# Performance work log

Hardware: AMD Instinct MI355X
Metric: run time of the kernel (lower is better)

The kernel has to match this reference:

```python
import jax, jax.numpy as jnp
import numpy as np

AVG_NOBJ = 49.0
NEG_SLOPE = 0.01  # torch leaky_relu default


def eops_1_to_2(x, nobj, aggregation):
    """x: [B,N,C] -> [B,C,5,N,N] equivariant basis (rank-1 -> rank-2)."""
    B, N, C = x.shape
    xt = jnp.transpose(x, (0, 2, 1))  # B,C,N
    if aggregation == 'sum':
        agg = xt.sum(-1) / AVG_NOBJ                      # B,C
    elif aggregation == 'mean':
        agg = xt.sum(-1) / nobj[:, None]                 # B,C
    elif aggregation == 'max':
        agg = xt.max(-1)
    elif aggregation == 'min':
        agg = xt.min(-1)
    eye = jnp.eye(N, dtype=x.dtype)                      # N,N
    op1 = xt[:, :, :, None] * eye                        # x_i on diagonal
    op2 = jnp.broadcast_to(xt[:, :, None, :], (B, C, N, N))  # x_j along rows
    op3 = jnp.broadcast_to(xt[:, :, :, None], (B, C, N, N))  # x_i along cols
    op4 = agg[:, :, None, None] * eye                    # agg on diagonal
    op5 = jnp.broadcast_to(agg[:, :, None, None], (B, C, N, N))  # agg everywhere
    return jnp.stack([op1, op2, op3, op4, op5], axis=2)  # B,C,5,N,N


def setup_inputs() -> dict:
    key = jax.random.key(0)
    k1, k2 = jax.random.split(key)
    B, N, C, S = 8, 128, 64, 64
    basis_total = 5 * 4  # 5 basis ops per config char, config='smxn'
    inputs = jax.random.normal(k1, (B, N, C), dtype=jnp.float32)
    mask = jnp.ones((B, N, N, 1), dtype=jnp.float32)
    nobj = jnp.full((B,), 100.0, dtype=jnp.float32)
    coefs = jax.random.normal(k2, (C, S, basis_total), dtype=jnp.float32) * np.sqrt(2.0 / (C * basis_total)).astype(np.float32)
    bias = jnp.zeros((S,), dtype=jnp.float32)
    return {"inputs": inputs, "mask": mask, "nobj": nobj, "coefs": coefs, "bias": bias}


def reference(inputs, mask, nobj, coefs, bias):
    # config = 'smxn' -> sum, mean, max, min basis tensors, concat on basis axis
    ops = jnp.concatenate(
        [eops_1_to_2(inputs, nobj, a) for a in ('sum', 'mean', 'max', 'min')],
        axis=2)  # B,C,20,N,N
    out = jnp.einsum('dsb,ndbij->nijs', coefs, ops)      # B,N,N,S
    out = out + bias[None, None, None, :]
    out = jnp.where(out >= 0, out, NEG_SLOPE * out)      # leaky_relu
    return out * mask
```

## Files before the change

### kernel.cpp

```cpp
#include <hip/hip_runtime.h>

constexpr int N = 128, S = 64;
constexpr float INV_AVG = 1.0f / 49.0f;
constexpr float SLOPE = 0.01f;

typedef float f4 __attribute__((ext_vector_type(4)));

__global__ __launch_bounds__(256) void fused_kernel(
    const float* __restrict__ x,
    const float* __restrict__ mask,
    const float* __restrict__ nobj,
    const float* __restrict__ coefs,
    const float* __restrict__ bias,
    float* __restrict__ out)
{
  __shared__ float xs[8192];
  __shared__ float w2[4096];
  __shared__ float ag[256];
  __shared__ float part[2560];
  __shared__ float fin[512];

  const int tid = threadIdx.x;
  const int n   = blockIdx.x >> 5;
  const int i0  = (blockIdx.x & 31) << 2;

  {
    const float4* xg = (const float4*)(x + n * N * 64);
    float4* xs4 = (float4*)xs;
#pragma unroll
    for (int k = 0; k < 8; ++k) xs4[tid + k * 256] = xg[tid + k * 256];
  }
  __syncthreads();

  {
    const int d = tid & 63, grp = tid >> 6;
    float sm = 0.f, mx = -INFINITY, mn = INFINITY;
    for (int i = grp * 32; i < grp * 32 + 32; ++i) {
      float v = xs[i * 64 + d];
      sm += v; mx = fmaxf(mx, v); mn = fminf(mn, v);
    }
    part[grp * 64 + d]       = sm;
    part[256 + grp * 64 + d] = mx;
    part[512 + grp * 64 + d] = mn;
  }
  __syncthreads();
  if (tid < 64) {
    float s0 = part[tid] + part[64 + tid] + part[128 + tid] + part[192 + tid];
    float m0 = fmaxf(fmaxf(part[256 + tid], part[320 + tid]),
                     fmaxf(part[384 + tid], part[448 + tid]));
    float n0 = fminf(fminf(part[512 + tid], part[576 + tid]),
                     fminf(part[640 + tid], part[704 + tid]));
    ag[tid]       = s0 * INV_AVG;
    ag[64 + tid]  = s0 / nobj[n];
    ag[128 + tid] = m0;
    ag[192 + tid] = n0;
  }
  __syncthreads();

  {
    const int g = tid >> 6;
    const int s = tid & 63;
    float pA[4] = {0,0,0,0}, pC[4] = {0,0,0,0};
    float pD = 0.f, pE = 0.f;
#pragma unroll
    for (int k = 0; k < 16; ++k) {
      const int e = k * 256 + tid;
      const int d = e >> 6;
      const float4* cp = (const float4*)(coefs + e * 20);
      float4 f0 = cp[0], f1 = cp[1], f2 = cp[2], f3 = cp[3], f4v = cp[4];
      float w1v = f0.x + f1.y + f2.z + f3.w;
      float w2v = f0.y + f1.z + f2.w + f4v.x;
      float w3v = f0.z + f1.w + f3.x + f4v.y;
      w2[e] = w2v;
#pragma unroll
      for (int m = 0; m < 4; ++m) {
        float xv = xs[(i0 + m) * 64 + d];
        pA[m] += xv * w1v;
        pC[m] += xv * w3v;
      }
      pD += ag[d] * f0.w + ag[64 + d] * f2.x + ag[128 + d] * f3.y + ag[192 + d] * f4v.z;
      pE += ag[d] * f1.x + ag[64 + d] * f2.y + ag[128 + d] * f3.z + ag[192 + d] * f4v.w;
    }
#pragma unroll
    for (int m = 0; m < 4; ++m) {
      part[m * 256 + g * 64 + s]       = pA[m];
      part[(4 + m) * 256 + g * 64 + s] = pC[m];
    }
    part[2048 + g * 64 + s] = pD;
    part[2304 + g * 64 + s] = pE;
  }
  __syncthreads();
  if (tid < 64) {
    const int s = tid;
    float D = part[2048 + s] + part[2048 + 64 + s] + part[2048 + 128 + s] + part[2048 + 192 + s];
    float E = part[2304 + s] + part[2304 + 64 + s] + part[2304 + 128 + s] + part[2304 + 192 + s];
    float bv = bias[s];
#pragma unroll
    for (int m = 0; m < 4; ++m) {
      float A = part[m * 256 + s] + part[m * 256 + 64 + s]
              + part[m * 256 + 128 + s] + part[m * 256 + 192 + s];
      float C = part[(4 + m) * 256 + s] + part[(4 + m) * 256 + 64 + s]
              + part[(4 + m) * 256 + 128 + s] + part[(4 + m) * 256 + 192 + s];
      fin[m * 64 + s]       = C + E + bv;
      fin[256 + m * 64 + s] = A + D;
    }
  }
  __syncthreads();

  const int l  = tid & 15;
  const int jg = tid >> 4;

  float4 base[4], diag[4];
#pragma unroll
  for (int m = 0; m < 4; ++m) {
    base[m] = *(const float4*)&fin[m * 64 + l * 4];
    diag[m] = *(const float4*)&fin[256 + m * 64 + l * 4];
  }

  float4 racc[8];
#pragma unroll
  for (int t = 0; t < 8; ++t) { racc[t].x = racc[t].y = racc[t].z = racc[t].w = 0.f; }

#pragma unroll 4
  for (int d = 0; d < 64; ++d) {
    float4 wq = *(const float4*)&w2[d * 64 + l * 4];
#pragma unroll
    for (int t = 0; t < 8; ++t) {
      float xv = xs[(jg + 16 * t) * 64 + d];
      racc[t].x += xv * wq.x;
      racc[t].y += xv * wq.y;
      racc[t].z += xv * wq.z;
      racc[t].w += xv * wq.w;
    }
  }

  f4* out4 = (f4*)out;
#pragma unroll
  for (int t = 0; t < 8; ++t) {
    const int j = jg + 16 * t;
#pragma unroll
    for (int m = 0; m < 4; ++m) {
      const int i = i0 + m;
      float v0 = base[m].x + racc[t].x;
      float v1 = base[m].y + racc[t].y;
      float v2 = base[m].z + racc[t].z;
      float v3 = base[m].w + racc[t].w;
      if (j == i) {
        v0 += diag[m].x; v1 += diag[m].y;
        v2 += diag[m].z; v3 += diag[m].w;
      }
      v0 = (v0 >= 0.f) ? v0 : SLOPE * v0;
      v1 = (v1 >= 0.f) ? v1 : SLOPE * v1;
      v2 = (v2 >= 0.f) ? v2 : SLOPE * v2;
      v3 = (v3 >= 0.f) ? v3 : SLOPE * v3;
      float mk = mask[(n * N + i) * N + j];
      f4 o;
      o.x = v0 * mk; o.y = v1 * mk; o.z = v2 * mk; o.w = v3 * mk;
      __builtin_nontemporal_store(o, &out4[(size_t)((n * N + i) * N + j) * 16 + l]);
    }
  }
}

extern "C" void kernel_launch(void* const* d_in, const int* in_sizes, int n_in,
                              void* d_out, int out_size, void* d_ws, size_t ws_size,
                              hipStream_t stream) {
  const float* x     = (const float*)d_in[0];
  const float* mask  = (const float*)d_in[1];
  const float* nobj  = (const float*)d_in[2];
  const float* coefs = (const float*)d_in[3];
  const float* bias  = (const float*)d_in[4];
  float* out = (float*)d_out;

  fused_kernel<<<256, 256, 0, stream>>>(x, mask, nobj, coefs, bias, out);
}
```

Measured before the change: 83.69 us.

## Swizzle shared x tile and vectorize inner GEMV loads across four d values

Stores the x tile in shared memory with a row-rotated float4 swizzle so that reading float4 chunks of different rows does not cause bank conflicts. The inner j-by-s accumulation now reads four consecutive d values per LDS and four w2 rows per step, which cuts shared-memory instruction count. The j-to-thread mapping is remapped so each wave covers a contiguous 32-row block. This changes the output write pattern and makes the reduction and coefficient phases use the swizzled indexing.

```diff
diff --git a/kernel.cpp b/kernel.cpp
--- a/kernel.cpp
+++ b/kernel.cpp
@@ -5,6 +5,13 @@
 constexpr float SLOPE = 0.01f;
 
 typedef float f4 __attribute__((ext_vector_type(4)));
+
+__device__ __forceinline__ int xs_q(int r, int qd) {
+  return r * 16 + ((qd + r) & 15);
+}
+__device__ __forceinline__ int xs_e(int r, int d) {
+  return r * 64 + 4 * (((d >> 2) + r) & 15) + (d & 3);
+}
 
 __global__ __launch_bounds__(256) void fused_kernel(
     const float* __restrict__ x,
@@ -28,7 +35,11 @@
     const float4* xg = (const float4*)(x + n * N * 64);
     float4* xs4 = (float4*)xs;
 #pragma unroll
-    for (int k = 0; k < 8; ++k) xs4[tid + k * 256] = xg[tid + k * 256];
+    for (int k = 0; k < 8; ++k) {
+      const int g = tid + k * 256;
+      const int r = g >> 4, q = g & 15;
+      xs4[xs_q(r, q)] = xg[g];
+    }
   }
   __syncthreads();
 
@@ -36,7 +47,7 @@
     const int d = tid & 63, grp = tid >> 6;
     float sm = 0.f, mx = -INFINITY, mn = INFINITY;
     for (int i = grp * 32; i < grp * 32 + 32; ++i) {
-      float v = xs[i * 64 + d];
+      float v = xs[xs_e(i, d)];
       sm += v; mx = fmaxf(mx, v); mn = fminf(mn, v);
     }
     part[grp * 64 + d]       = sm;
@@ -74,7 +85,7 @@
       w2[e] = w2v;
 #pragma unroll
       for (int m = 0; m < 4; ++m) {
-        float xv = xs[(i0 + m) * 64 + d];
+        float xv = xs[xs_e(i0 + m, d)];
         pA[m] += xv * w1v;
         pC[m] += xv * w3v;
       }
@@ -107,8 +118,9 @@
   }
   __syncthreads();
 
+  const int w  = tid >> 6;
+  const int jb = (tid >> 4) & 3;
   const int l  = tid & 15;
-  const int jg = tid >> 4;
 
   float4 base[4], diag[4];
 #pragma unroll
@@ -122,22 +134,26 @@
   for (int t = 0; t < 8; ++t) { racc[t].x = racc[t].y = racc[t].z = racc[t].w = 0.f; }
 
 #pragma unroll 4
-  for (int d = 0; d < 64; ++d) {
-    float4 wq = *(const float4*)&w2[d * 64 + l * 4];
+  for (int qd = 0; qd < 16; ++qd) {
+    float4 wq0 = *(const float4*)&w2[(4 * qd + 0) * 64 + l * 4];
+    float4 wq1 = *(const float4*)&w2[(4 * qd + 1) * 64 + l * 4];
+    float4 wq2 = *(const float4*)&w2[(4 * qd + 2) * 64 + l * 4];
+    float4 wq3 = *(const float4*)&w2[(4 * qd + 3) * 64 + l * 4];
 #pragma unroll
     for (int t = 0; t < 8; ++t) {
-      float xv = xs[(jg + 16 * t) * 64 + d];
-      racc[t].x += xv * wq.x;
-      racc[t].y += xv * wq.y;
-      racc[t].z += xv * wq.z;
-      racc[t].w += xv * wq.w;
+      const int j = w * 32 + 4 * t + jb;
+      float4 xv = *(const float4*)&xs[4 * xs_q(j, qd)];
+      racc[t].x += xv.x * wq0.x + xv.y * wq1.x + xv.z * wq2.x + xv.w * wq3.x;
+      racc[t].y += xv.x * wq0.y + xv.y * wq1.y + xv.z * wq2.y + xv.w * wq3.y;
+      racc[t].z += xv.x * wq0.z + xv.y * wq1.z + xv.z * wq2.z + xv.w * wq3.z;
+      racc[t].w += xv.x * wq0.w + xv.y * wq1.w + xv.z * wq2.w + xv.w * wq3.w;
     }
   }
 
   f4* out4 = (f4*)out;
 #pragma unroll
   for (int t = 0; t < 8; ++t) {
-    const int j = jg + 16 * t;
+    const int j = w * 32 + 4 * t + jb;
 #pragma unroll
     for (int m = 0; m < 4; ++m) {
       const int i = i0 + m;
```

New measurement: 86.25 us. +3.1%, slower.

## Split into prep and elementwise assemble kernels with precomputed row projections

Applied to the files above, without the earlier changes.

Moves the per-row x·w2 projection into a prep kernel that computes it once per (n,row) and stores base, diagonal and row terms in workspace. A separate wide elementwise kernel then combines them with mask and leaky_relu, one float4 per thread. This removes the redundant GEMM that every block previously recomputed and raises parallelism for the output write. It adds a second launch and a workspace round trip, and drops the nontemporal stores.

```diff
diff --git a/kernel.cpp b/kernel.cpp
--- a/kernel.cpp
+++ b/kernel.cpp
@@ -4,21 +4,20 @@
 constexpr float INV_AVG = 1.0f / 49.0f;
 constexpr float SLOPE = 0.01f;
 
-typedef float f4 __attribute__((ext_vector_type(4)));
+constexpr int WS_BASE = 0;
+constexpr int WS_DIAG = 65536;
+constexpr int WS_R    = 131072;
 
-__global__ __launch_bounds__(256) void fused_kernel(
+__global__ __launch_bounds__(256) void prep_kernel(
     const float* __restrict__ x,
-    const float* __restrict__ mask,
     const float* __restrict__ nobj,
     const float* __restrict__ coefs,
     const float* __restrict__ bias,
-    float* __restrict__ out)
+    float* __restrict__ ws)
 {
   __shared__ float xs[8192];
-  __shared__ float w2[4096];
   __shared__ float ag[256];
-  __shared__ float part[2560];
-  __shared__ float fin[512];
+  __shared__ float part[3584];
 
   const int tid = threadIdx.x;
   const int n   = blockIdx.x >> 5;
@@ -60,7 +59,7 @@
   {
     const int g = tid >> 6;
     const int s = tid & 63;
-    float pA[4] = {0,0,0,0}, pC[4] = {0,0,0,0};
+    float pA[4] = {0,0,0,0}, pR[4] = {0,0,0,0}, pC[4] = {0,0,0,0};
     float pD = 0.f, pE = 0.f;
 #pragma unroll
     for (int k = 0; k < 16; ++k) {
@@ -71,11 +70,11 @@
       float w1v = f0.x + f1.y + f2.z + f3.w;
       float w2v = f0.y + f1.z + f2.w + f4v.x;
       float w3v = f0.z + f1.w + f3.x + f4v.y;
-      w2[e] = w2v;
 #pragma unroll
       for (int m = 0; m < 4; ++m) {
         float xv = xs[(i0 + m) * 64 + d];
         pA[m] += xv * w1v;
+        pR[m] += xv * w2v;
         pC[m] += xv * w3v;
       }
       pD += ag[d] * f0.w + ag[64 + d] * f2.x + ag[128 + d] * f3.y + ag[192 + d] * f4v.z;
@@ -83,17 +82,21 @@
     }
 #pragma unroll
     for (int m = 0; m < 4; ++m) {
-      part[m * 256 + g * 64 + s]       = pA[m];
-      part[(4 + m) * 256 + g * 64 + s] = pC[m];
+      part[m * 256 + g * 64 + s]        = pA[m];
+      part[(4 + m) * 256 + g * 64 + s]  = pC[m];
+      part[(8 + m) * 256 + g * 64 + s]  = pR[m];
     }
-    part[2048 + g * 64 + s] = pD;
-    part[2304 + g * 64 + s] = pE;
+    part[3072 + g * 64 + s] = pD;
+    part[3328 + g * 64 + s] = pE;
   }
   __syncthreads();
+
   if (tid < 64) {
     const int s = tid;
-    float D = part[2048 + s] + part[2048 + 64 + s] + part[2048 + 128 + s] + part[2048 + 192 + s];
-    float E = part[2304 + s] + part[2304 + 64 + s] + part[2304 + 128 + s] + part[2304 + 192 + s];
+    float D = part[3072 + s] + part[3072 + 64 + s]
+            + part[3072 + 128 + s] + part[3072 + 192 + s];
+    float E = part[3328 + s] + part[3328 + 64 + s]
+            + part[3328 + 128 + s] + part[3328 + 192 + s];
     float bv = bias[s];
 #pragma unroll
     for (int m = 0; m < 4; ++m) {
@@ -101,64 +104,53 @@
               + part[m * 256 + 128 + s] + part[m * 256 + 192 + s];
       float C = part[(4 + m) * 256 + s] + part[(4 + m) * 256 + 64 + s]
               + part[(4 + m) * 256 + 128 + s] + part[(4 + m) * 256 + 192 + s];
-      fin[m * 64 + s]       = C + E + bv;
-      fin[256 + m * 64 + s] = A + D;
+      float R = part[(8 + m) * 256 + s] + part[(8 + m) * 256 + 64 + s]
+              + part[(8 + m) * 256 + 128 + s] + part[(8 + m) * 256 + 192 + s];
+      const int o = (n * N + i0 + m) * 64 + s;
+      ws[WS_BASE + o] = C + E + bv;
+      ws[WS_DIAG + o] = A + D;
+      ws[WS_R    + o] = R;
     }
   }
-  __syncthreads();
+}
 
-  const int l  = tid & 15;
-  const int jg = tid >> 4;
+__global__ __launch_bounds__(256) void assemble_kernel(
+    const float* __restrict__ ws,
+    const float* __restrict__ mask,
+    float* __restrict__ out)
+{
+  const int g  = blockIdx.x * 256 + threadIdx.x;
+  const int l  = g & 15;
+  const int p  = g >> 4;
+  const int j  = p & 127;
+  const int bi = p >> 7;
+  const int i  = bi & 127;
+  const int n  = bi >> 7;
 
-  float4 base[4], diag[4];
-#pragma unroll
-  for (int m = 0; m < 4; ++m) {
-    base[m] = *(const float4*)&fin[m * 64 + l * 4];
-    diag[m] = *(const float4*)&fin[256 + m * 64 + l * 4];
+  const float4* B4 = (const float4*)(ws + WS_BASE);
+  const float4* G4 = (const float4*)(ws + WS_DIAG);
+  const float4* R4 = (const float4*)(ws + WS_R);
+
+  float4 b = B4[bi * 16 + l];
+  float4 r = R4[(n * N + j) * 16 + l];
+  float mk = mask[p];
+
+  float v0 = b.x + r.x;
+  float v1 = b.y + r.y;
+  float v2 = b.z + r.z;
+  float v3 = b.w + r.w;
+  if (i == j) {
+    float4 dg = G4[bi * 16 + l];
+    v0 += dg.x; v1 += dg.y; v2 += dg.z; v3 += dg.w;
   }
+  v0 = (v0 >= 0.f) ? v0 : SLOPE * v0;
+  v1 = (v1 >= 0.f) ? v1 : SLOPE * v1;
+  v2 = (v2 >= 0.f) ? v2 : SLOPE * v2;
+  v3 = (v3 >= 0.f) ? v3 : SLOPE * v3;
 
-  float4 racc[8];
-#pragma unroll
-  for (int t = 0; t < 8; ++t) { racc[t].x = racc[t].y = racc[t].z = racc[t].w = 0.f; }
-
-#pragma unroll 4
-  for (int d = 0; d < 64; ++d) {
-    float4 wq = *(const float4*)&w2[d * 64 + l * 4];
-#pragma unroll
-    for (int t = 0; t < 8; ++t) {
-      float xv = xs[(jg + 16 * t) * 64 + d];
-      racc[t].x += xv * wq.x;
-      racc[t].y += xv * wq.y;
-      racc[t].z += xv * wq.z;
-      racc[t].w += xv * wq.w;
-    }
-  }
-
-  f4* out4 = (f4*)out;
-#pragma unroll
-  for (int t = 0; t < 8; ++t) {
-    const int j = jg + 16 * t;
-#pragma unroll
-    for (int m = 0; m < 4; ++m) {
-      const int i = i0 + m;
-      float v0 = base[m].x + racc[t].x;
-      float v1 = base[m].y + racc[t].y;
-      float v2 = base[m].z + racc[t].z;
-      float v3 = base[m].w + racc[t].w;
-      if (j == i) {
-        v0 += diag[m].x; v1 += diag[m].y;
-        v2 += diag[m].z; v3 += diag[m].w;
-      }
-      v0 = (v0 >= 0.f) ? v0 : SLOPE * v0;
-      v1 = (v1 >= 0.f) ? v1 : SLOPE * v1;
-      v2 = (v2 >= 0.f) ? v2 : SLOPE * v2;
-      v3 = (v3 >= 0.f) ? v3 : SLOPE * v3;
-      float mk = mask[(n * N + i) * N + j];
-      f4 o;
-      o.x = v0 * mk; o.y = v1 * mk; o.z = v2 * mk; o.w = v3 * mk;
-      __builtin_nontemporal_store(o, &out4[(size_t)((n * N + i) * N + j) * 16 + l]);
-    }
-  }
+  float4 o;
+  o.x = v0 * mk; o.y = v1 * mk; o.z = v2 * mk; o.w = v3 * mk;
+  ((float4*)out)[g] = o;
 }
 
 extern "C" void kernel_launch(void* const* d_in, const int* in_sizes, int n_in,
@@ -170,6 +162,8 @@
   const float* coefs = (const float*)d_in[3];
   const float* bias  = (const float*)d_in[4];
   float* out = (float*)d_out;
+  float* ws  = (float*)d_ws;
 
-  fused_kernel<<<256, 256, 0, stream>>>(x, mask, nobj, coefs, bias, out);
+  prep_kernel<<<256, 256, 0, stream>>>(x, nobj, coefs, bias, ws);
+  assemble_kernel<<<8192, 256, 0, stream>>>(ws, mask, out);
 }
```

Result: faster. 81.39 us (-2.7%).
